# Performance work log

Hardware: AMD Instinct MI355X
Metric: run time of the kernel (lower is better)

## Reference

```python
import jax, jax.numpy as jnp
import numpy as np

N_NODES = 100000
N_EDGES = 400000
N_GRAPHS = 2000
IN_DIM = 58
HEADS = 4
HID = 64           # per-head hidden = output_dim // heads = 256 // 4
OUT = 256
NEG_SLOPE = 0.2    # PyG GATConv default


def _glorot(key, shape):
    fan_in, fan_out = shape[0], shape[-1]
    lim = jnp.sqrt(6.0 / (fan_in + fan_out)).astype(jnp.float32)
    return jax.random.uniform(key, shape, jnp.float32, -lim, lim)


def setup_inputs() -> dict:
    key = jax.random.key(0)
    ks = jax.random.split(key, 16)
    x = jax.random.normal(ks[0], (N_NODES, IN_DIM), jnp.float32)
    edge_index = jax.random.randint(ks[1], (2, N_EDGES), 0, N_NODES, jnp.int64)
    batch = jnp.sort(jax.random.randint(ks[2], (N_NODES,), 0, N_GRAPHS, jnp.int64))
    return {
        "x": x,
        "edge_index": edge_index,
        "batch": batch,
        # layer 1: 58 -> 4 heads x 64, concat -> 256
        "W1": _glorot(ks[3], (IN_DIM, HEADS * HID)),
        "a_src1": _glorot(ks[4], (HEADS, HID)),
        "a_dst1": _glorot(ks[5], (HEADS, HID)),
        "b1": jnp.zeros((HEADS * HID,), jnp.float32),
        # layer 2: 256 -> 4 heads x 64, concat -> 256
        "W2": _glorot(ks[6], (HEADS * HID, HEADS * HID)),
        "a_src2": _glorot(ks[7], (HEADS, HID)),
        "a_dst2": _glorot(ks[8], (HEADS, HID)),
        "b2": jnp.zeros((HEADS * HID,), jnp.float32),
        # layer 3: 256 -> 1 head x 256, no concat (mean over 1 head)
        "W3": _glorot(ks[9], (HEADS * HID, OUT)),
        "a_src3": _glorot(ks[10], (1, OUT)),
        "a_dst3": _glorot(ks[11], (1, OUT)),
        "b3": jnp.zeros((OUT,), jnp.float32),
    }


def _gat_layer(x, src, dst, W, a_src, a_dst, b, heads, ch, concat):
    n = x.shape[0]
    h = (x @ W).reshape(n, heads, ch)                      # [N,H,C]
    e_src = jnp.einsum("nhc,hc->nh", h, a_src)             # [N,H]
    e_dst = jnp.einsum("nhc,hc->nh", h, a_dst)
    e = jax.nn.leaky_relu(e_src[src] + e_dst[dst], NEG_SLOPE)  # [E,H]
    # segment softmax over destination nodes (self-loops ensure non-empty segments)
    m = jax.ops.segment_max(e, dst, num_segments=n)
    ex = jnp.exp(e - m[dst])
    denom = jax.ops.segment_sum(ex, dst, num_segments=n)
    coef = ex / denom[dst]                                 # [E,H]
    out = jax.ops.segment_sum(h[src] * coef[:, :, None], dst, num_segments=n)
    out = out.reshape(n, heads * ch) if concat else out.mean(axis=1)
    return out + b


def reference(x, edge_index, batch, W1, a_src1, a_dst1, b1,
              W2, a_src2, a_dst2, b2, W3, a_src3, a_dst3, b3):
    n = x.shape[0]
    loops = jnp.arange(n, dtype=edge_index.dtype)
    src = jnp.concatenate([edge_index[0], loops])          # add_self_loops (PyG default)
    dst = jnp.concatenate([edge_index[1], loops])
    h = jax.nn.relu(_gat_layer(x, src, dst, W1, a_src1, a_dst1, b1, HEADS, HID, True))
    h = jax.nn.relu(_gat_layer(h, src, dst, W2, a_src2, a_dst2, b2, HEADS, HID, True))
    h = _gat_layer(h, src, dst, W3, a_src3, a_dst3, b3, 1, OUT, False)
    # global max pool over graphs
    return jax.ops.segment_max(h, batch, num_segments=N_GRAPHS)
```

## Files before the change

kernel.cpp:

```cpp
#include <hip/hip_runtime.h>
#include <hip/hip_bf16.h>
#include <math.h>

#define N_NODES_C 100000
#define E_ORIG    400000
#define E_TOT     500000
#define N_GRAPHS_C 2000
#define KDIM      256

typedef __attribute__((ext_vector_type(8))) short short8v;
typedef __attribute__((ext_vector_type(4))) float f32x4;

__device__ __forceinline__ void gload_lds16(const void* g, void* l) {
    __builtin_amdgcn_global_load_lds(
        (const __attribute__((address_space(1))) unsigned int*)g,
        (__attribute__((address_space(3))) unsigned int*)l, 16, 0, 0);
}

__device__ __forceinline__ float bflo(unsigned u) { return __uint_as_float(u << 16); }
__device__ __forceinline__ float bfhi(unsigned u) { return __uint_as_float(u & 0xffff0000u); }

__global__ void count_deg_k(const int* __restrict__ ei, int* __restrict__ deg) {
    int e = blockIdx.x * 256 + threadIdx.x;
    if (e >= E_TOT) return;
    int d = (e < E_ORIG) ? ei[E_ORIG + e] : (e - E_ORIG);
    atomicAdd(&deg[d], 1);
}

__global__ void scan_chunk(const int* __restrict__ in, int* __restrict__ out,
                           int* __restrict__ partials, int n) {
    __shared__ int s[256];
    int tid = threadIdx.x;
    int i = blockIdx.x * 256 + tid;
    int v = (i < n) ? in[i] : 0;
    s[tid] = v;
    __syncthreads();
    for (int off = 1; off < 256; off <<= 1) {
        int t = (tid >= off) ? s[tid - off] : 0;
        __syncthreads();
        s[tid] += t;
        __syncthreads();
    }
    if (i < n) out[i] = s[tid] - v;
    if (tid == 255) partials[blockIdx.x] = s[255];
}

__global__ void scan_partials(int* p, int nb) {
    __shared__ int s[512];
    int tid = threadIdx.x;
    int v = (tid < nb) ? p[tid] : 0;
    s[tid] = v;
    __syncthreads();
    for (int off = 1; off < 512; off <<= 1) {
        int t = (tid >= off) ? s[tid - off] : 0;
        __syncthreads();
        s[tid] += t;
        __syncthreads();
    }
    if (tid < nb) p[tid] = s[tid] - v;
}

__global__ void add_partials(int* out, const int* __restrict__ p, int n) {
    int i = blockIdx.x * 256 + threadIdx.x;
    if (i < n) out[i] += p[blockIdx.x];
}

__global__ void scatter_k(const int* __restrict__ ei, const int* __restrict__ rowoff,
                          int* cursor, int* __restrict__ csr_src,
                          int* __restrict__ csr_dst) {
    int e = blockIdx.x * 256 + threadIdx.x;
    if (e >= E_TOT) return;
    int s, d;
    if (e < E_ORIG) { s = ei[e]; d = ei[E_ORIG + e]; }
    else            { s = e - E_ORIG; d = s; }
    int pos = rowoff[d] + atomicAdd(&cursor[d], 1);
    csr_src[pos] = s;
    csr_dst[pos] = d;
}

__global__ void conv_x_k(const float* __restrict__ x, __hip_bfloat16* __restrict__ Xb) {
    int idx = blockIdx.x * 256 + threadIdx.x;
    if (idx >= N_NODES_C * 64) return;
    int row = idx >> 6, c = idx & 63;
    float v = (c < 58) ? x[row * 58 + c] : 0.f;
    Xb[idx] = __float2bfloat16(v);
}

template <int K, int KPAD>
__global__ void conv_wt_k(const float* __restrict__ W, __hip_bfloat16* __restrict__ Wt) {
    int idx = blockIdx.x * 256 + threadIdx.x;
    if (idx >= 256 * KPAD) return;
    int c = idx / KPAD, k = idx - c * KPAD;
    float v = (k < K) ? W[k * 256 + c] : 0.f;
    Wt[idx] = __float2bfloat16(v);
}

template <int KPAD, int NH>
__global__ __launch_bounds__(256, 2) void gemm_mfma(
        const __hip_bfloat16* __restrict__ Xb, const __hip_bfloat16* __restrict__ Wt,
        const float* __restrict__ ASRC, const float* __restrict__ ADST,
        __hip_bfloat16* __restrict__ H, float* __restrict__ ES, float* __restrict__ ED) {
    __shared__ char As[128 * 128];
    __shared__ char Bs[256 * 128];
    __shared__ float red[2][128][2];

    const int t = threadIdx.x;
    const int wv = t >> 6, lane = t & 63;
    const int wr = wv >> 1, wc = wv & 1;
    const int r15 = lane & 15, hi = lane >> 4;
    const int n0 = blockIdx.x * 128;
    const int srow = lane >> 3;
    const int sx = ((lane & 7) ^ srow) * 16;
    constexpr int KB = KPAD * 2;

    f32x4 acc[4][8];
#pragma unroll
    for (int m = 0; m < 4; m++)
#pragma unroll
        for (int n = 0; n < 8; n++) acc[m][n] = (f32x4){0.f, 0.f, 0.f, 0.f};

    for (int kt = 0; kt < KPAD / 64; kt++) {
        if (kt) __syncthreads();
        const int k0b = kt * 128;
#pragma unroll
        for (int p = 0; p < 4; p++) {
            int i = wv * 4 + p;
            int gr = n0 + i * 8 + srow;
            if (gr > N_NODES_C - 1) gr = N_NODES_C - 1;
            gload_lds16((const char*)Xb + (size_t)gr * KB + k0b + sx, As + i * 1024);
        }
#pragma unroll
        for (int p = 0; p < 8; p++) {
            int i = wv * 8 + p;
            int col = i * 8 + srow;
            gload_lds16((const char*)Wt + (size_t)col * KB + k0b + sx, Bs + i * 1024);
        }
        asm volatile("s_waitcnt vmcnt(0)" ::: "memory");
        __syncthreads();

#pragma unroll
        for (int ks = 0; ks < 2; ks++) {
            const int cx = ((ks * 4 + hi) ^ (r15 & 7)) * 16;
            short8v a[4];
#pragma unroll
            for (int m = 0; m < 4; m++)
                a[m] = *(const short8v*)(As + (wr * 64 + m * 16 + r15) * 128 + cx);
#pragma unroll
            for (int n = 0; n < 8; n++) {
                short8v b = *(const short8v*)(Bs + (wc * 128 + n * 16 + r15) * 128 + cx);
#pragma unroll
                for (int m = 0; m < 4; m++)
                    acc[m][n] = __builtin_amdgcn_mfma_f32_16x16x32_bf16(a[m], b, acc[m][n], 0, 0, 0);
            }
        }
    }

    float asv[8], adv[8];
#pragma unroll
    for (int n = 0; n < 8; n++) {
        int col = wc * 128 + n * 16 + r15;
        asv[n] = ASRC[col];
        adv[n] = ADST[col];
    }

#pragma unroll
    for (int m = 0; m < 4; m++) {
#pragma unroll
        for (int j = 0; j < 4; j++) {
            int lrow = wr * 64 + m * 16 + hi * 4 + j;
            int row = n0 + lrow;
            bool ok = row < N_NODES_C;
            if (ok) {
#pragma unroll
                for (int n = 0; n < 8; n++)
                    H[(size_t)row * KDIM + wc * 128 + n * 16 + r15] =
                        __float2bfloat16(acc[m][n][j]);
            }
            if (NH == 4) {
                float p0s = 0.f, p1s = 0.f, p0d = 0.f, p1d = 0.f;
#pragma unroll
                for (int n = 0; n < 4; n++) {
                    p0s = fmaf(acc[m][n][j], asv[n], p0s);
                    p0d = fmaf(acc[m][n][j], adv[n], p0d);
                    p1s = fmaf(acc[m][n + 4][j], asv[n + 4], p1s);
                    p1d = fmaf(acc[m][n + 4][j], adv[n + 4], p1d);
                }
#pragma unroll
                for (int s = 8; s; s >>= 1) {
                    p0s += __shfl_xor(p0s, s, 16);
                    p0d += __shfl_xor(p0d, s, 16);
                    p1s += __shfl_xor(p1s, s, 16);
                    p1d += __shfl_xor(p1d, s, 16);
                }
                if (r15 == 0 && ok) {
                    ES[row * 4 + wc * 2 + 0] = p0s;
                    ES[row * 4 + wc * 2 + 1] = p1s;
                    ED[row * 4 + wc * 2 + 0] = p0d;
                    ED[row * 4 + wc * 2 + 1] = p1d;
                }
            } else {
                float ps = 0.f, pd = 0.f;
#pragma unroll
                for (int n = 0; n < 8; n++) {
                    ps = fmaf(acc[m][n][j], asv[n], ps);
                    pd = fmaf(acc[m][n][j], adv[n], pd);
                }
#pragma unroll
                for (int s = 8; s; s >>= 1) {
                    ps += __shfl_xor(ps, s, 16);
                    pd += __shfl_xor(pd, s, 16);
                }
                if (r15 == 0) { red[0][lrow][wc] = ps; red[1][lrow][wc] = pd; }
            }
        }
    }
    if (NH == 1) {
        __syncthreads();
        if (t < 128) {
            int row = n0 + t;
            if (row < N_NODES_C) {
                ES[row] = red[0][t][0] + red[0][t][1];
                ED[row] = red[1][t][0] + red[1][t][1];
            }
        }
    }
}

template <int NH>
__global__ __launch_bounds__(256) void edge_e_k(
        const int* __restrict__ csr_src, const int* __restrict__ csr_dst,
        const float* __restrict__ ES, const float* __restrict__ ED,
        float* __restrict__ E) {
    int j = blockIdx.x * 256 + threadIdx.x;
    if (j >= E_TOT) return;
    int s = csr_src[j], d = csr_dst[j];
    if (NH == 4) {
        float4 es = *(const float4*)&ES[s * 4];
        float4 ed = *(const float4*)&ED[d * 4];
        float4 e;
        e.x = es.x + ed.x; e.x = (e.x > 0.f) ? e.x : 0.2f * e.x;
        e.y = es.y + ed.y; e.y = (e.y > 0.f) ? e.y : 0.2f * e.y;
        e.z = es.z + ed.z; e.z = (e.z > 0.f) ? e.z : 0.2f * e.z;
        e.w = es.w + ed.w; e.w = (e.w > 0.f) ? e.w : 0.2f * e.w;
        *(float4*)&E[j * 4] = e;
    } else {
        float e = ES[s] + ED[d];
        E[j] = (e > 0.f) ? e : 0.2f * e;
    }
}

template <int NH, bool RELU>
__global__ __launch_bounds__(256) void agg_kernel(
        const __hip_bfloat16* __restrict__ H, const int* __restrict__ rowoff,
        const int* __restrict__ csr_src, const float* __restrict__ E,
        const float* __restrict__ bias, __hip_bfloat16* __restrict__ Out) {
    int node = blockIdx.x * 8 + (threadIdx.x >> 5);
    int l = threadIdx.x & 31;
    int c0 = l * 8;
    int head = (NH == 4) ? (l >> 3) : 0;
    int beg = rowoff[node], end = rowoff[node + 1];

    float m = -1e30f;
    for (int j = beg; j < end; j++) m = fmaxf(m, E[j * NH + head]);

    float s = 0.f;
    float a[8];
#pragma unroll
    for (int i = 0; i < 8; i++) a[i] = 0.f;
    const unsigned short* Hu = (const unsigned short*)H;

#define ACC8(v, p) \
    a[0] = fmaf(p, bflo(v.x), a[0]); a[1] = fmaf(p, bfhi(v.x), a[1]); \
    a[2] = fmaf(p, bflo(v.y), a[2]); a[3] = fmaf(p, bfhi(v.y), a[3]); \
    a[4] = fmaf(p, bflo(v.z), a[4]); a[5] = fmaf(p, bfhi(v.z), a[5]); \
    a[6] = fmaf(p, bflo(v.w), a[6]); a[7] = fmaf(p, bfhi(v.w), a[7]);

    int j = beg;
    for (; j + 4 <= end; j += 4) {
        int s0 = csr_src[j], s1 = csr_src[j + 1], s2 = csr_src[j + 2], s3 = csr_src[j + 3];
        float e0 = E[(j + 0) * NH + head], e1 = E[(j + 1) * NH + head];
        float e2 = E[(j + 2) * NH + head], e3 = E[(j + 3) * NH + head];
        uint4 v0 = *(const uint4*)(Hu + (size_t)s0 * KDIM + c0);
        uint4 v1 = *(const uint4*)(Hu + (size_t)s1 * KDIM + c0);
        uint4 v2 = *(const uint4*)(Hu + (size_t)s2 * KDIM + c0);
        uint4 v3 = *(const uint4*)(Hu + (size_t)s3 * KDIM + c0);
        float p0 = __expf(e0 - m), p1 = __expf(e1 - m);
        float p2 = __expf(e2 - m), p3 = __expf(e3 - m);
        s += p0 + p1 + p2 + p3;
        ACC8(v0, p0)
        ACC8(v1, p1)
        ACC8(v2, p2)
        ACC8(v3, p3)
    }
    for (; j < end; j++) {
        int s0 = csr_src[j];
        float e0 = E[j * NH + head];
        uint4 v0 = *(const uint4*)(Hu + (size_t)s0 * KDIM + c0);
        float p0 = __expf(e0 - m);
        s += p0;
        ACC8(v0, p0)
    }
#undef ACC8

    float inv = 1.f / s;
    float4 b0 = *(const float4*)&bias[c0];
    float4 b1 = *(const float4*)&bias[c0 + 4];
    float o[8];
    o[0] = fmaf(a[0], inv, b0.x); o[1] = fmaf(a[1], inv, b0.y);
    o[2] = fmaf(a[2], inv, b0.z); o[3] = fmaf(a[3], inv, b0.w);
    o[4] = fmaf(a[4], inv, b1.x); o[5] = fmaf(a[5], inv, b1.y);
    o[6] = fmaf(a[6], inv, b1.z); o[7] = fmaf(a[7], inv, b1.w);
    __hip_bfloat16 rb[8];
#pragma unroll
    for (int i = 0; i < 8; i++) {
        float v = RELU ? fmaxf(o[i], 0.f) : o[i];
        rb[i] = __float2bfloat16(v);
    }
    *(uint4*)&Out[(size_t)node * KDIM + c0] = *(uint4*)rb;
}

__global__ __launch_bounds__(256) void pool_k(
        const __hip_bfloat16* __restrict__ O, const int* __restrict__ batch,
        float* __restrict__ out) {
    __shared__ int range[2];
    __shared__ float red[3][256];
    int g = blockIdx.x, k = threadIdx.x;
    if (k < 2) {
        int v = g + k;
        int lo = 0, hi = N_NODES_C;
        while (lo < hi) { int mid = (lo + hi) >> 1; if (batch[mid] < v) lo = mid + 1; else hi = mid; }
        range[k] = lo;
    }
    __syncthreads();
    int cg = k & 63;
    int ro = k >> 6;
    float m0 = -INFINITY, m1 = -INFINITY, m2 = -INFINITY, m3 = -INFINITY;
    const unsigned short* Ou = (const unsigned short*)O;
    for (int i = range[0] + ro; i < range[1]; i += 4) {
        uint2 v = *(const uint2*)(Ou + (size_t)i * KDIM + cg * 4);
        m0 = fmaxf(m0, bflo(v.x)); m1 = fmaxf(m1, bfhi(v.x));
        m2 = fmaxf(m2, bflo(v.y)); m3 = fmaxf(m3, bfhi(v.y));
    }
    if (ro) {
        red[ro - 1][cg * 4 + 0] = m0; red[ro - 1][cg * 4 + 1] = m1;
        red[ro - 1][cg * 4 + 2] = m2; red[ro - 1][cg * 4 + 3] = m3;
    }
    __syncthreads();
    if (ro == 0) {
        m0 = fmaxf(fmaxf(m0, red[0][cg * 4 + 0]), fmaxf(red[1][cg * 4 + 0], red[2][cg * 4 + 0]));
        m1 = fmaxf(fmaxf(m1, red[0][cg * 4 + 1]), fmaxf(red[1][cg * 4 + 1], red[2][cg * 4 + 1]));
        m2 = fmaxf(fmaxf(m2, red[0][cg * 4 + 2]), fmaxf(red[1][cg * 4 + 2], red[2][cg * 4 + 2]));
        m3 = fmaxf(fmaxf(m3, red[0][cg * 4 + 3]), fmaxf(red[1][cg * 4 + 3], red[2][cg * 4 + 3]));
        float4 o = make_float4(m0, m1, m2, m3);
        *(float4*)&out[(size_t)g * KDIM + cg * 4] = o;
    }
}

extern "C" void kernel_launch(void* const* d_in, const int* in_sizes, int n_in,
                              void* d_out, int out_size, void* d_ws, size_t ws_size,
                              hipStream_t stream) {
    const float* x     = (const float*)d_in[0];
    const int*   ei    = (const int*)d_in[1];
    const int*   batch = (const int*)d_in[2];
    const float* W1  = (const float*)d_in[3];
    const float* as1 = (const float*)d_in[4];
    const float* ad1 = (const float*)d_in[5];
    const float* b1  = (const float*)d_in[6];
    const float* W2  = (const float*)d_in[7];
    const float* as2 = (const float*)d_in[8];
    const float* ad2 = (const float*)d_in[9];
    const float* b2  = (const float*)d_in[10];
    const float* W3  = (const float*)d_in[11];
    const float* as3 = (const float*)d_in[12];
    const float* ad3 = (const float*)d_in[13];
    const float* b3  = (const float*)d_in[14];
    float* out = (float*)d_out;

    char* p = (char*)d_ws;
    auto alloc = [&](size_t bytes) { char* r = p; p += (bytes + 255) & ~(size_t)255; return r; };
    __hip_bfloat16* Xb  = (__hip_bfloat16*)alloc((size_t)N_NODES_C * 64 * 2);
    __hip_bfloat16* Hb  = (__hip_bfloat16*)alloc((size_t)N_NODES_C * KDIM * 2);
    __hip_bfloat16* Nb  = (__hip_bfloat16*)alloc((size_t)N_NODES_C * KDIM * 2);
    __hip_bfloat16* Wt1 = (__hip_bfloat16*)alloc(256 * 64 * 2);
    __hip_bfloat16* Wt2 = (__hip_bfloat16*)alloc(256 * 256 * 2);
    __hip_bfloat16* Wt3 = (__hip_bfloat16*)alloc(256 * 256 * 2);
    float* ES     = (float*)alloc((size_t)N_NODES_C * 4 * 4);
    float* ED     = (float*)alloc((size_t)N_NODES_C * 4 * 4);
    float* Ecoef  = (float*)alloc((size_t)E_TOT * 4 * 4);
    int* deg      = (int*)alloc((N_NODES_C + 1) * 4);
    int* rowoff   = (int*)alloc((N_NODES_C + 1) * 4);
    int* cursor   = (int*)alloc(N_NODES_C * 4);
    int* csr      = (int*)alloc((size_t)E_TOT * 4 + 256);
    int* csrd     = (int*)alloc((size_t)E_TOT * 4);
    int* partials = (int*)alloc(512 * 4);

    conv_x_k<<<(N_NODES_C * 64 + 255) / 256, 256, 0, stream>>>(x, Xb);
    conv_wt_k<58, 64><<<64, 256, 0, stream>>>(W1, Wt1);
    conv_wt_k<256, 256><<<256, 256, 0, stream>>>(W2, Wt2);
    conv_wt_k<256, 256><<<256, 256, 0, stream>>>(W3, Wt3);

    hipMemsetAsync(deg, 0, (N_NODES_C + 1) * 4, stream);
    hipMemsetAsync(cursor, 0, N_NODES_C * 4, stream);
    int egrid = (E_TOT + 255) / 256;
    count_deg_k<<<egrid, 256, 0, stream>>>(ei, deg);
    int nb = (N_NODES_C + 1 + 255) / 256;
    scan_chunk<<<nb, 256, 0, stream>>>(deg, rowoff, partials, N_NODES_C + 1);
    scan_partials<<<1, 512, 0, stream>>>(partials, nb);
    add_partials<<<nb, 256, 0, stream>>>(rowoff, partials, N_NODES_C + 1);
    scatter_k<<<egrid, 256, 0, stream>>>(ei, rowoff, cursor, csr, csrd);

    int ggrid = (N_NODES_C + 127) / 128;
    int agrid = N_NODES_C / 8;
    gemm_mfma<64, 4><<<ggrid, 256, 0, stream>>>(Xb, Wt1, as1, ad1, Hb, ES, ED);
    edge_e_k<4><<<egrid, 256, 0, stream>>>(csr, csrd, ES, ED, Ecoef);
    agg_kernel<4, true><<<agrid, 256, 0, stream>>>(Hb, rowoff, csr, Ecoef, b1, Nb);
    gemm_mfma<256, 4><<<ggrid, 256, 0, stream>>>(Nb, Wt2, as2, ad2, Hb, ES, ED);
    edge_e_k<4><<<egrid, 256, 0, stream>>>(csr, csrd, ES, ED, Ecoef);
    agg_kernel<4, true><<<agrid, 256, 0, stream>>>(Hb, rowoff, csr, Ecoef, b2, Nb);
    gemm_mfma<256, 1><<<ggrid, 256, 0, stream>>>(Nb, Wt3, as3, ad3, Hb, ES, ED);
    edge_e_k<1><<<egrid, 256, 0, stream>>>(csr, csrd, ES, ED, Ecoef);
    agg_kernel<1, false><<<agrid, 256, 0, stream>>>(Hb, rowoff, csr, Ecoef, b3, Nb);
    pool_k<<<N_GRAPHS_C, 256, 0, stream>>>(Nb, batch, out);
}
```

Before: 341.7 us.

## Fuse conversion launches, merge memsets, and use 16 lanes per node in aggregation

```diff
diff --git a/kernel.cpp b/kernel.cpp
--- a/kernel.cpp
+++ b/kernel.cpp
@@ -78,21 +78,33 @@
     csr_dst[pos] = d;
 }
 
-__global__ void conv_x_k(const float* __restrict__ x, __hip_bfloat16* __restrict__ Xb) {
+#define XE  (N_NODES_C * 64)
+#define W1E (256 * 64)
+#define WBE (256 * 256)
+__global__ __launch_bounds__(256) void conv_all_k(
+        const float* __restrict__ x, const float* __restrict__ W1,
+        const float* __restrict__ W2, const float* __restrict__ W3,
+        __hip_bfloat16* __restrict__ Xb, __hip_bfloat16* __restrict__ Wt1,
+        __hip_bfloat16* __restrict__ Wt2, __hip_bfloat16* __restrict__ Wt3) {
     int idx = blockIdx.x * 256 + threadIdx.x;
-    if (idx >= N_NODES_C * 64) return;
-    int row = idx >> 6, c = idx & 63;
-    float v = (c < 58) ? x[row * 58 + c] : 0.f;
-    Xb[idx] = __float2bfloat16(v);
-}
-
-template <int K, int KPAD>
-__global__ void conv_wt_k(const float* __restrict__ W, __hip_bfloat16* __restrict__ Wt) {
-    int idx = blockIdx.x * 256 + threadIdx.x;
-    if (idx >= 256 * KPAD) return;
-    int c = idx / KPAD, k = idx - c * KPAD;
-    float v = (k < K) ? W[k * 256 + c] : 0.f;
-    Wt[idx] = __float2bfloat16(v);
+    if (idx < XE) {
+        int row = idx >> 6, c = idx & 63;
+        float v = (c < 58) ? x[row * 58 + c] : 0.f;
+        Xb[idx] = __float2bfloat16(v);
+    } else if (idx < XE + W1E) {
+        int i = idx - XE;
+        int c = i >> 6, k = i & 63;
+        float v = (k < 58) ? W1[k * 256 + c] : 0.f;
+        Wt1[i] = __float2bfloat16(v);
+    } else if (idx < XE + W1E + WBE) {
+        int i = idx - XE - W1E;
+        int c = i >> 8, k = i & 255;
+        Wt2[i] = __float2bfloat16(W2[k * 256 + c]);
+    } else if (idx < XE + W1E + 2 * WBE) {
+        int i = idx - XE - W1E - WBE;
+        int c = i >> 8, k = i & 255;
+        Wt3[i] = __float2bfloat16(W3[k * 256 + c]);
+    }
 }
 
 template <int KPAD, int NH>
@@ -254,69 +266,83 @@
         const __hip_bfloat16* __restrict__ H, const int* __restrict__ rowoff,
         const int* __restrict__ csr_src, const float* __restrict__ E,
         const float* __restrict__ bias, __hip_bfloat16* __restrict__ Out) {
-    int node = blockIdx.x * 8 + (threadIdx.x >> 5);
-    int l = threadIdx.x & 31;
-    int c0 = l * 8;
-    int head = (NH == 4) ? (l >> 3) : 0;
+    int node = blockIdx.x * 16 + (threadIdx.x >> 4);
+    int l = threadIdx.x & 15;
+    int c0 = l * 16;
+    int head = (NH == 4) ? (l >> 2) : 0;
     int beg = rowoff[node], end = rowoff[node + 1];
 
     float m = -1e30f;
     for (int j = beg; j < end; j++) m = fmaxf(m, E[j * NH + head]);
 
     float s = 0.f;
-    float a[8];
-#pragma unroll
-    for (int i = 0; i < 8; i++) a[i] = 0.f;
+    float a[16];
+#pragma unroll
+    for (int i = 0; i < 16; i++) a[i] = 0.f;
     const unsigned short* Hu = (const unsigned short*)H;
 
-#define ACC8(v, p) \
-    a[0] = fmaf(p, bflo(v.x), a[0]); a[1] = fmaf(p, bfhi(v.x), a[1]); \
-    a[2] = fmaf(p, bflo(v.y), a[2]); a[3] = fmaf(p, bfhi(v.y), a[3]); \
-    a[4] = fmaf(p, bflo(v.z), a[4]); a[5] = fmaf(p, bfhi(v.z), a[5]); \
-    a[6] = fmaf(p, bflo(v.w), a[6]); a[7] = fmaf(p, bfhi(v.w), a[7]);
+#define ACCV(va, vb, p) \
+    a[0]  = fmaf(p, bflo(va.x), a[0]);  a[1]  = fmaf(p, bfhi(va.x), a[1]); \
+    a[2]  = fmaf(p, bflo(va.y), a[2]);  a[3]  = fmaf(p, bfhi(va.y), a[3]); \
+    a[4]  = fmaf(p, bflo(va.z), a[4]);  a[5]  = fmaf(p, bfhi(va.z), a[5]); \
+    a[6]  = fmaf(p, bflo(va.w), a[6]);  a[7]  = fmaf(p, bfhi(va.w), a[7]); \
+    a[8]  = fmaf(p, bflo(vb.x), a[8]);  a[9]  = fmaf(p, bfhi(vb.x), a[9]); \
+    a[10] = fmaf(p, bflo(vb.y), a[10]); a[11] = fmaf(p, bfhi(vb.y), a[11]); \
+    a[12] = fmaf(p, bflo(vb.z), a[12]); a[13] = fmaf(p, bfhi(vb.z), a[13]); \
+    a[14] = fmaf(p, bflo(vb.w), a[14]); a[15] = fmaf(p, bfhi(vb.w), a[15]);
 
     int j = beg;
     for (; j + 4 <= end; j += 4) {
         int s0 = csr_src[j], s1 = csr_src[j + 1], s2 = csr_src[j + 2], s3 = csr_src[j + 3];
         float e0 = E[(j + 0) * NH + head], e1 = E[(j + 1) * NH + head];
         float e2 = E[(j + 2) * NH + head], e3 = E[(j + 3) * NH + head];
-        uint4 v0 = *(const uint4*)(Hu + (size_t)s0 * KDIM + c0);
-        uint4 v1 = *(const uint4*)(Hu + (size_t)s1 * KDIM + c0);
-        uint4 v2 = *(const uint4*)(Hu + (size_t)s2 * KDIM + c0);
-        uint4 v3 = *(const uint4*)(Hu + (size_t)s3 * KDIM + c0);
+        uint4 v0a = *(const uint4*)(Hu + (size_t)s0 * KDIM + c0);
+        uint4 v0b = *(const uint4*)(Hu + (size_t)s0 * KDIM + c0 + 8);
+        uint4 v1a = *(const uint4*)(Hu + (size_t)s1 * KDIM + c0);
+        uint4 v1b = *(const uint4*)(Hu + (size_t)s1 * KDIM + c0 + 8);
+        uint4 v2a = *(const uint4*)(Hu + (size_t)s2 * KDIM + c0);
+        uint4 v2b = *(const uint4*)(Hu + (size_t)s2 * KDIM + c0 + 8);
+        uint4 v3a = *(const uint4*)(Hu + (size_t)s3 * KDIM + c0);
+        uint4 v3b = *(const uint4*)(Hu + (size_t)s3 * KDIM + c0 + 8);
         float p0 = __expf(e0 - m), p1 = __expf(e1 - m);
         float p2 = __expf(e2 - m), p3 = __expf(e3 - m);
         s += p0 + p1 + p2 + p3;
-        ACC8(v0, p0)
-        ACC8(v1, p1)
-        ACC8(v2, p2)
-        ACC8(v3, p3)
+        ACCV(v0a, v0b, p0)
+        ACCV(v1a, v1b, p1)
+        ACCV(v2a, v2b, p2)
+        ACCV(v3a, v3b, p3)
     }
     for (; j < end; j++) {
         int s0 = csr_src[j];
         float e0 = E[j * NH + head];
-        uint4 v0 = *(const uint4*)(Hu + (size_t)s0 * KDIM + c0);
+        uint4 va = *(const uint4*)(Hu + (size_t)s0 * KDIM + c0);
+        uint4 vb = *(const uint4*)(Hu + (size_t)s0 * KDIM + c0 + 8);
         float p0 = __expf(e0 - m);
         s += p0;
-        ACC8(v0, p0)
-    }
-#undef ACC8
+        ACCV(va, vb, p0)
+    }
+#undef ACCV
 
     float inv = 1.f / s;
-    float4 b0 = *(const float4*)&bias[c0];
-    float4 b1 = *(const float4*)&bias[c0 + 4];
-    float o[8];
-    o[0] = fmaf(a[0], inv, b0.x); o[1] = fmaf(a[1], inv, b0.y);
-    o[2] = fmaf(a[2], inv, b0.z); o[3] = fmaf(a[3], inv, b0.w);
-    o[4] = fmaf(a[4], inv, b1.x); o[5] = fmaf(a[5], inv, b1.y);
-    o[6] = fmaf(a[6], inv, b1.z); o[7] = fmaf(a[7], inv, b1.w);
-    __hip_bfloat16 rb[8];
-#pragma unroll
-    for (int i = 0; i < 8; i++) {
-        float v = RELU ? fmaxf(o[i], 0.f) : o[i];
-        rb[i] = __float2bfloat16(v);
-    }
-    *(uint4*)&Out[(size_t)node * KDIM + c0] = *(uint4*)rb;
+    __hip_bfloat16 rb[16];
+#pragma unroll
+    for (int q = 0; q < 4; q++) {
+        float4 b4 = *(const float4*)&bias[c0 + q * 4];
+        float o0 = fmaf(a[q * 4 + 0], inv, b4.x);
+        float o1 = fmaf(a[q * 4 + 1], inv, b4.y);
+        float o2 = fmaf(a[q * 4 + 2], inv, b4.z);
+        float o3 = fmaf(a[q * 4 + 3], inv, b4.w);
+        if (RELU) {
+            o0 = fmaxf(o0, 0.f); o1 = fmaxf(o1, 0.f);
+            o2 = fmaxf(o2, 0.f); o3 = fmaxf(o3, 0.f);
+        }
+        rb[q * 4 + 0] = __float2bfloat16(o0);
+        rb[q * 4 + 1] = __float2bfloat16(o1);
+        rb[q * 4 + 2] = __float2bfloat16(o2);
+        rb[q * 4 + 3] = __float2bfloat16(o3);
+    }
+    *(uint4*)&Out[(size_t)node * KDIM + c0] = *(uint4*)&rb[0];
+    *(uint4*)&Out[(size_t)node * KDIM + c0 + 8] = *(uint4*)&rb[8];
 }
 
 __global__ __launch_bounds__(256) void pool_k(
@@ -387,20 +413,18 @@
     float* ES     = (float*)alloc((size_t)N_NODES_C * 4 * 4);
     float* ED     = (float*)alloc((size_t)N_NODES_C * 4 * 4);
     float* Ecoef  = (float*)alloc((size_t)E_TOT * 4 * 4);
-    int* deg      = (int*)alloc((N_NODES_C + 1) * 4);
+    int* degcur   = (int*)alloc((size_t)(2 * N_NODES_C + 1) * 4);
+    int* deg      = degcur;
+    int* cursor   = degcur + (N_NODES_C + 1);
     int* rowoff   = (int*)alloc((N_NODES_C + 1) * 4);
-    int* cursor   = (int*)alloc(N_NODES_C * 4);
     int* csr      = (int*)alloc((size_t)E_TOT * 4 + 256);
     int* csrd     = (int*)alloc((size_t)E_TOT * 4);
     int* partials = (int*)alloc(512 * 4);
 
-    conv_x_k<<<(N_NODES_C * 64 + 255) / 256, 256, 0, stream>>>(x, Xb);
-    conv_wt_k<58, 64><<<64, 256, 0, stream>>>(W1, Wt1);
-    conv_wt_k<256, 256><<<256, 256, 0, stream>>>(W2, Wt2);
-    conv_wt_k<256, 256><<<256, 256, 0, stream>>>(W3, Wt3);
-
-    hipMemsetAsync(deg, 0, (N_NODES_C + 1) * 4, stream);
-    hipMemsetAsync(cursor, 0, N_NODES_C * 4, stream);
+    int ctot = XE + W1E + 2 * WBE;
+    conv_all_k<<<(ctot + 255) / 256, 256, 0, stream>>>(x, W1, W2, W3, Xb, Wt1, Wt2, Wt3);
+
+    hipMemsetAsync(degcur, 0, (size_t)(2 * N_NODES_C + 1) * 4, stream);
     int egrid = (E_TOT + 255) / 256;
     count_deg_k<<<egrid, 256, 0, stream>>>(ei, deg);
     int nb = (N_NODES_C + 1 + 255) / 256;
@@ -410,7 +434,7 @@
     scatter_k<<<egrid, 256, 0, stream>>>(ei, rowoff, cursor, csr, csrd);
 
     int ggrid = (N_NODES_C + 127) / 128;
-    int agrid = N_NODES_C / 8;
+    int agrid = N_NODES_C / 16;
     gemm_mfma<64, 4><<<ggrid, 256, 0, stream>>>(Xb, Wt1, as1, ad1, Hb, ES, ED);
     edge_e_k<4><<<egrid, 256, 0, stream>>>(csr, csrd, ES, ED, Ecoef);
     agg_kernel<4, true><<<agrid, 256, 0, stream>>>(Hb, rowoff, csr, Ecoef, b1, Nb);
```

Result: no change. 342.0 us (+0.1%).

## Fuse edge-score computation into aggregation and merge preprocessing kernels

Applied to the files above, without the earlier changes.

```diff
diff --git a/kernel.cpp b/kernel.cpp
--- a/kernel.cpp
+++ b/kernel.cpp
@@ -20,11 +20,39 @@
 __device__ __forceinline__ float bflo(unsigned u) { return __uint_as_float(u << 16); }
 __device__ __forceinline__ float bfhi(unsigned u) { return __uint_as_float(u & 0xffff0000u); }
 
-__global__ void count_deg_k(const int* __restrict__ ei, int* __restrict__ deg) {
-    int e = blockIdx.x * 256 + threadIdx.x;
-    if (e >= E_TOT) return;
-    int d = (e < E_ORIG) ? ei[E_ORIG + e] : (e - E_ORIG);
-    atomicAdd(&deg[d], 1);
+#define XE  (N_NODES_C * 64)
+#define W1E (256 * 64)
+#define WBE (256 * 256)
+__global__ __launch_bounds__(256) void conv_all_count(
+        const float* __restrict__ x, const float* __restrict__ W1,
+        const float* __restrict__ W2, const float* __restrict__ W3,
+        const int* __restrict__ ei,
+        __hip_bfloat16* __restrict__ Xb, __hip_bfloat16* __restrict__ Wt1,
+        __hip_bfloat16* __restrict__ Wt2, __hip_bfloat16* __restrict__ Wt3,
+        int* __restrict__ deg) {
+    int idx = blockIdx.x * 256 + threadIdx.x;
+    if (idx < E_TOT) {
+        int d = (idx < E_ORIG) ? ei[E_ORIG + idx] : (idx - E_ORIG);
+        atomicAdd(&deg[d], 1);
+    }
+    if (idx < XE) {
+        int row = idx >> 6, c = idx & 63;
+        float v = (c < 58) ? x[row * 58 + c] : 0.f;
+        Xb[idx] = __float2bfloat16(v);
+    } else if (idx < XE + W1E) {
+        int i = idx - XE;
+        int c = i >> 6, k = i & 63;
+        float v = (k < 58) ? W1[k * 256 + c] : 0.f;
+        Wt1[i] = __float2bfloat16(v);
+    } else if (idx < XE + W1E + WBE) {
+        int i = idx - XE - W1E;
+        int c = i >> 8, k = i & 255;
+        Wt2[i] = __float2bfloat16(W2[k * 256 + c]);
+    } else if (idx < XE + W1E + 2 * WBE) {
+        int i = idx - XE - W1E - WBE;
+        int c = i >> 8, k = i & 255;
+        Wt3[i] = __float2bfloat16(W3[k * 256 + c]);
+    }
 }
 
 __global__ void scan_chunk(const int* __restrict__ in, int* __restrict__ out,
@@ -45,24 +73,20 @@
     if (tid == 255) partials[blockIdx.x] = s[255];
 }
 
-__global__ void scan_partials(int* p, int nb) {
-    __shared__ int s[512];
-    int tid = threadIdx.x;
-    int v = (tid < nb) ? p[tid] : 0;
-    s[tid] = v;
-    __syncthreads();
-    for (int off = 1; off < 512; off <<= 1) {
-        int t = (tid >= off) ? s[tid - off] : 0;
+__global__ void scan_fix(int* __restrict__ rowoff, const int* __restrict__ partials, int n) {
+    __shared__ int sred[256];
+    int t = threadIdx.x;
+    int acc = 0;
+    for (int i = t; i < blockIdx.x; i += 256) acc += partials[i];
+    sred[t] = acc;
+    __syncthreads();
+    for (int off = 128; off; off >>= 1) {
+        if (t < off) sred[t] += sred[t + off];
         __syncthreads();
-        s[tid] += t;
-        __syncthreads();
-    }
-    if (tid < nb) p[tid] = s[tid] - v;
-}
-
-__global__ void add_partials(int* out, const int* __restrict__ p, int n) {
-    int i = blockIdx.x * 256 + threadIdx.x;
-    if (i < n) out[i] += p[blockIdx.x];
+    }
+    int base = sred[0];
+    int i = blockIdx.x * 256 + t;
+    if (i < n) rowoff[i] += base;
 }
 
 __global__ void scatter_k(const int* __restrict__ ei, const int* __restrict__ rowoff,
@@ -76,23 +100,6 @@
     int pos = rowoff[d] + atomicAdd(&cursor[d], 1);
     csr_src[pos] = s;
     csr_dst[pos] = d;
-}
-
-__global__ void conv_x_k(const float* __restrict__ x, __hip_bfloat16* __restrict__ Xb) {
-    int idx = blockIdx.x * 256 + threadIdx.x;
-    if (idx >= N_NODES_C * 64) return;
-    int row = idx >> 6, c = idx & 63;
-    float v = (c < 58) ? x[row * 58 + c] : 0.f;
-    Xb[idx] = __float2bfloat16(v);
-}
-
-template <int K, int KPAD>
-__global__ void conv_wt_k(const float* __restrict__ W, __hip_bfloat16* __restrict__ Wt) {
-    int idx = blockIdx.x * 256 + threadIdx.x;
-    if (idx >= 256 * KPAD) return;
-    int c = idx / KPAD, k = idx - c * KPAD;
-    float v = (k < K) ? W[k * 256 + c] : 0.f;
-    Wt[idx] = __float2bfloat16(v);
 }
 
 template <int KPAD, int NH>
@@ -226,42 +233,61 @@
     }
 }
 
-template <int NH>
-__global__ __launch_bounds__(256) void edge_e_k(
-        const int* __restrict__ csr_src, const int* __restrict__ csr_dst,
-        const float* __restrict__ ES, const float* __restrict__ ED,
-        float* __restrict__ E) {
-    int j = blockIdx.x * 256 + threadIdx.x;
-    if (j >= E_TOT) return;
-    int s = csr_src[j], d = csr_dst[j];
-    if (NH == 4) {
-        float4 es = *(const float4*)&ES[s * 4];
-        float4 ed = *(const float4*)&ED[d * 4];
-        float4 e;
-        e.x = es.x + ed.x; e.x = (e.x > 0.f) ? e.x : 0.2f * e.x;
-        e.y = es.y + ed.y; e.y = (e.y > 0.f) ? e.y : 0.2f * e.y;
-        e.z = es.z + ed.z; e.z = (e.z > 0.f) ? e.z : 0.2f * e.z;
-        e.w = es.w + ed.w; e.w = (e.w > 0.f) ? e.w : 0.2f * e.w;
-        *(float4*)&E[j * 4] = e;
-    } else {
-        float e = ES[s] + ED[d];
-        E[j] = (e > 0.f) ? e : 0.2f * e;
-    }
-}
-
+#define ECAP 160
 template <int NH, bool RELU>
 __global__ __launch_bounds__(256) void agg_kernel(
         const __hip_bfloat16* __restrict__ H, const int* __restrict__ rowoff,
-        const int* __restrict__ csr_src, const float* __restrict__ E,
+        const int* __restrict__ csr_src, const int* __restrict__ csr_dst,
+        const float* __restrict__ ES, const float* __restrict__ ED,
         const float* __restrict__ bias, __hip_bfloat16* __restrict__ Out) {
-    int node = blockIdx.x * 8 + (threadIdx.x >> 5);
-    int l = threadIdx.x & 31;
+    __shared__ float Els[ECAP * NH];
+    __shared__ int   Sls[ECAP];
+    __shared__ int   roff[9];
+    int t = threadIdx.x;
+    int n0 = blockIdx.x * 8;
+    if (t < 9) roff[t] = rowoff[n0 + t];
+    __syncthreads();
+    int beg0 = roff[0];
+    int ne = roff[8] - beg0;
+    int nl = (ne < ECAP) ? ne : ECAP;
+    for (int j = t; j < nl; j += 256) {
+        int slot = beg0 + j;
+        int srcj = csr_src[slot];
+        int dj   = csr_dst[slot];
+        Sls[j] = srcj;
+        if (NH == 4) {
+            float4 es = *(const float4*)&ES[srcj * 4];
+            float4 ed = *(const float4*)&ED[dj * 4];
+            float e;
+            e = es.x + ed.x; Els[j * 4 + 0] = (e > 0.f) ? e : 0.2f * e;
+            e = es.y + ed.y; Els[j * 4 + 1] = (e > 0.f) ? e : 0.2f * e;
+            e = es.z + ed.z; Els[j * 4 + 2] = (e > 0.f) ? e : 0.2f * e;
+            e = es.w + ed.w; Els[j * 4 + 3] = (e > 0.f) ? e : 0.2f * e;
+        } else {
+            float e = ES[srcj] + ED[dj];
+            Els[j] = (e > 0.f) ? e : 0.2f * e;
+        }
+    }
+    __syncthreads();
+
+    int g = t >> 5;
+    int node = n0 + g;
+    int l = t & 31;
     int c0 = l * 8;
     int head = (NH == 4) ? (l >> 3) : 0;
-    int beg = rowoff[node], end = rowoff[node + 1];
+    int jb = roff[g] - beg0, je = roff[g + 1] - beg0;
+    int jeF = (je < ECAP) ? je : ECAP;
 
     float m = -1e30f;
-    for (int j = beg; j < end; j++) m = fmaxf(m, E[j * NH + head]);
+    for (int j = jb; j < jeF; j++) m = fmaxf(m, Els[j * NH + head]);
+    if (je > ECAP) {
+        float edv = ED[node * NH + head];
+        for (int j = ECAP; j < je; j++) {
+            float e = ES[csr_src[beg0 + j] * NH + head] + edv;
+            e = (e > 0.f) ? e : 0.2f * e;
+            m = fmaxf(m, e);
+        }
+    }
 
     float s = 0.f;
     float a[8];
@@ -275,11 +301,11 @@
     a[4] = fmaf(p, bflo(v.z), a[4]); a[5] = fmaf(p, bfhi(v.z), a[5]); \
     a[6] = fmaf(p, bflo(v.w), a[6]); a[7] = fmaf(p, bfhi(v.w), a[7]);
 
-    int j = beg;
-    for (; j + 4 <= end; j += 4) {
-        int s0 = csr_src[j], s1 = csr_src[j + 1], s2 = csr_src[j + 2], s3 = csr_src[j + 3];
-        float e0 = E[(j + 0) * NH + head], e1 = E[(j + 1) * NH + head];
-        float e2 = E[(j + 2) * NH + head], e3 = E[(j + 3) * NH + head];
+    int j = jb;
+    for (; j + 4 <= jeF; j += 4) {
+        int s0 = Sls[j], s1 = Sls[j + 1], s2 = Sls[j + 2], s3 = Sls[j + 3];
+        float e0 = Els[(j + 0) * NH + head], e1 = Els[(j + 1) * NH + head];
+        float e2 = Els[(j + 2) * NH + head], e3 = Els[(j + 3) * NH + head];
         uint4 v0 = *(const uint4*)(Hu + (size_t)s0 * KDIM + c0);
         uint4 v1 = *(const uint4*)(Hu + (size_t)s1 * KDIM + c0);
         uint4 v2 = *(const uint4*)(Hu + (size_t)s2 * KDIM + c0);
@@ -292,13 +318,25 @@
         ACC8(v2, p2)
         ACC8(v3, p3)
     }
-    for (; j < end; j++) {
-        int s0 = csr_src[j];
-        float e0 = E[j * NH + head];
+    for (; j < jeF; j++) {
+        int s0 = Sls[j];
+        float e0 = Els[j * NH + head];
         uint4 v0 = *(const uint4*)(Hu + (size_t)s0 * KDIM + c0);
         float p0 = __expf(e0 - m);
         s += p0;
         ACC8(v0, p0)
+    }
+    if (je > ECAP) {
+        float edv = ED[node * NH + head];
+        for (int jj = ECAP; jj < je; jj++) {
+            int sj = csr_src[beg0 + jj];
+            float e = ES[sj * NH + head] + edv;
+            e = (e > 0.f) ? e : 0.2f * e;
+            float p = __expf(e - m);
+            s += p;
+            uint4 v = *(const uint4*)(Hu + (size_t)sj * KDIM + c0);
+            ACC8(v, p)
+        }
     }
 #undef ACC8
 
@@ -386,39 +424,32 @@
     __hip_bfloat16* Wt3 = (__hip_bfloat16*)alloc(256 * 256 * 2);
     float* ES     = (float*)alloc((size_t)N_NODES_C * 4 * 4);
     float* ED     = (float*)alloc((size_t)N_NODES_C * 4 * 4);
-    float* Ecoef  = (float*)alloc((size_t)E_TOT * 4 * 4);
-    int* deg      = (int*)alloc((N_NODES_C + 1) * 4);
+    int* degcur   = (int*)alloc((size_t)(2 * N_NODES_C + 1) * 4);
+    int* deg      = degcur;
+    int* cursor   = degcur + (N_NODES_C + 1);
     int* rowoff   = (int*)alloc((N_NODES_C + 1) * 4);
-    int* cursor   = (int*)alloc(N_NODES_C * 4);
     int* csr      = (int*)alloc((size_t)E_TOT * 4 + 256);
     int* csrd     = (int*)alloc((size_t)E_TOT * 4);
     int* partials = (int*)alloc(512 * 4);
 
-    conv_x_k<<<(N_NODES_C * 64 + 255) / 256, 256, 0, stream>>>(x, Xb);
-    conv_wt_k<58, 64><<<64, 256, 0, stream>>>(W1, Wt1);
-    conv_wt_k<256, 256><<<256, 256, 0, stream>>>(W2, Wt2);
-    conv_wt_k<256, 256><<<256, 256, 0, stream>>>(W3, Wt3);
-
-    hipMemsetAsync(deg, 0, (N_NODES_C + 1) * 4, stream);
-    hipMemsetAsync(cursor, 0, N_NODES_C * 4, stream);
-    int egrid = (E_TOT + 255) / 256;
-    count_deg_k<<<egrid, 256, 0, stream>>>(ei, deg);
+    hipMemsetAsync(degcur, 0, (size_t)(2 * N_NODES_C + 1) * 4, stream);
+    int ctot = XE + W1E + 2 * WBE;
+    conv_all_count<<<(ctot + 255) / 256, 256, 0, stream>>>(
+        x, W1, W2, W3, ei, Xb, Wt1, Wt2, Wt3, deg);
+
     int nb = (N_NODES_C + 1 + 255) / 256;
     scan_chunk<<<nb, 256, 0, stream>>>(deg, rowoff, partials, N_NODES_C + 1);
-    scan_partials<<<1, 512, 0, stream>>>(partials, nb);
-    add_partials<<<nb, 256, 0, stream>>>(rowoff, partials, N_NODES_C + 1);
+    scan_fix<<<nb, 256, 0, stream>>>(rowoff, partials, N_NODES_C + 1);
+    int egrid = (E_TOT + 255) / 256;
     scatter_k<<<egrid, 256, 0, stream>>>(ei, rowoff, cursor, csr, csrd);
 
     int ggrid = (N_NODES_C + 127) / 128;
     int agrid = N_NODES_C / 8;
     gemm_mfma<64, 4><<<ggrid, 256, 0, stream>>>(Xb, Wt1, as1, ad1, Hb, ES, ED);
-    edge_e_k<4><<<egrid, 256, 0, stream>>>(csr, csrd, ES, ED, Ecoef);
-    agg_kernel<4, true><<<agrid, 256, 0, stream>>>(Hb, rowoff, csr, Ecoef, b1, Nb);
+    agg_kernel<4, true><<<agrid, 256, 0, stream>>>(Hb, rowoff, csr, csrd, ES, ED, b1, Nb);
     gemm_mfma<256, 4><<<ggrid, 256, 0, stream>>>(Nb, Wt2, as2, ad2, Hb, ES, ED);
-    edge_e_k<4><<<egrid, 256, 0, stream>>>(csr, csrd, ES, ED, Ecoef);
-    agg_kernel<4, true><<<agrid, 256, 0, stream>>>(Hb, rowoff, csr, Ecoef, b2, Nb);
+    agg_kernel<4, true><<<agrid, 256, 0, stream>>>(Hb, rowoff, csr, csrd, ES, ED, b2, Nb);
     gemm_mfma<256, 1><<<ggrid, 256, 0, stream>>>(Nb, Wt3, as3, ad3, Hb, ES, ED);
-    edge_e_k<1><<<egrid, 256, 0, stream>>>(csr, csrd, ES, ED, Ecoef);
-    agg_kernel<1, false><<<agrid, 256, 0, stream>>>(Hb, rowoff, csr, Ecoef, b3, Nb);
+    agg_kernel<1, false><<<agrid, 256, 0, stream>>>(Hb, rowoff, csr, csrd, ES, ED, b3, Nb);
     pool_k<<<N_GRAPHS_C, 256, 0, stream>>>(Nb, batch, out);
 }
```

Result: faster. 318.1 us (-6.9%).
